# Kernel tuning notes

Measured on AMD Instinct MI355X. Metric: run time of the kernel, lower is better.

## Reference

```python
import jax, jax.numpy as jnp
import numpy as np

G_NUM, K_DEG = 3, 3  # grid intervals, spline order (module defaults)
LN_EPS = 1e-5


def _bspline_basis(x, grid, k):
    """Cox-de Boor B-spline basis. x: [N, D], grid: [D, G+2k+1] -> [N, D, G+k]."""
    xg = x[:, :, None]                      # [N, D, 1]
    g = grid[None, :, :]                    # [1, D, M]
    B = ((xg >= g[..., :-1]) & (xg < g[..., 1:])).astype(x.dtype)  # degree 0
    for d in range(1, k + 1):
        left = (xg - g[..., :-(d + 1)]) / (g[..., d:-1] - g[..., :-(d + 1)])
        right = (g[..., d + 1:] - xg) / (g[..., d + 1:] - g[..., 1:-d])
        B = left * B[..., :-1] + right * B[..., 1:]
    return B                                # [N, D, G+k]


def _kan_layer(x, grid, coef, scale_base, scale_sp, node_scale, node_bias):
    # spline branch: fold per-edge scale_sp into coef, contract basis without
    # materializing the [N, in, out] per-edge tensor
    basis = _bspline_basis(x, grid, K_DEG)              # [N, in, G+k]
    coef_eff = coef * scale_sp[..., None]               # [in, out, G+k]
    y = jnp.einsum('nib,iob->no', basis, coef_eff)      # spline sum over edges
    y = y + jax.nn.silu(x) @ scale_base                 # residual base function
    return node_scale * y + node_bias                   # per-node affine


def setup_inputs() -> dict:
    key = jax.random.key(0)
    ks = jax.random.split(key, 12)
    B, S = 16, 1024
    D0, D1, D2 = 256, 512, 256
    nb = G_NUM + K_DEG  # num basis fns = 6
    h = 2.0 / G_NUM
    knots = np.arange(-K_DEG, G_NUM + K_DEG + 1) * h - 1.0  # [G+2k+1]=10, range [-3,3]
    grid1 = jnp.asarray(np.tile(knots, (D0, 1)), jnp.float32)
    grid2 = jnp.asarray(np.tile(knots, (D1, 1)), jnp.float32)
    inp = {
        'x': jax.random.normal(ks[0], (B, S, D0), jnp.float32),
        'grid1': grid1,
        'coef1': jax.random.normal(ks[1], (D0, D1, nb), jnp.float32) * 0.1,
        'scale_base1': jax.random.normal(ks[2], (D0, D1), jnp.float32) / np.sqrt(D0),
        'scale_sp1': jnp.ones((D0, D1), jnp.float32),
        'node_scale1': jnp.ones((D1,), jnp.float32),
        'node_bias1': jnp.zeros((D1,), jnp.float32),
        'grid2': grid2,
        'coef2': jax.random.normal(ks[3], (D1, D2, nb), jnp.float32) * 0.1,
        'scale_base2': jax.random.normal(ks[4], (D1, D2), jnp.float32) / np.sqrt(D1),
        'scale_sp2': jnp.ones((D1, D2), jnp.float32),
        'node_scale2': jnp.ones((D2,), jnp.float32),
        'node_bias2': jnp.zeros((D2,), jnp.float32),
        'ln_gamma': jnp.ones((D2,), jnp.float32),
        'ln_beta': jnp.zeros((D2,), jnp.float32),
    }
    return inp


def reference(x, grid1, coef1, scale_base1, scale_sp1, node_scale1, node_bias1,
              grid2, coef2, scale_base2, scale_sp2, node_scale2, node_bias2,
              ln_gamma, ln_beta):
    b, s, d = x.shape
    residual = x  # start_dim == final_dim -> residual path active
    h = x.reshape(-1, d)
    h = _kan_layer(h, grid1, coef1, scale_base1, scale_sp1, node_scale1, node_bias1)
    h = _kan_layer(h, grid2, coef2, scale_base2, scale_sp2, node_scale2, node_bias2)
    h = h.reshape(b, s, -1)
    h = h + residual
    # LayerNorm over last dim
    mu = jnp.mean(h, axis=-1, keepdims=True)
    var = jnp.mean((h - mu) ** 2, axis=-1, keepdims=True)
    h = (h - mu) * jax.lax.rsqrt(var + LN_EPS) * ln_gamma + ln_beta
    # torch nn.GELU default is exact (erf) variant
    return jax.nn.gelu(h, approximate=False)
```

## Files before the change

kernel.cpp:

```cpp
#include <hip/hip_runtime.h>
#include <cstdint>
#include <cstddef>

using f16   = _Float16;
using half8 = __attribute__((ext_vector_type(8))) _Float16;
using f32x4 = __attribute__((ext_vector_type(4))) float;
using ull   = unsigned long long;

#define DINL __device__ __forceinline__

DINL void gload_lds16(const void* gptr, void* lptr) {
  __builtin_amdgcn_global_load_lds(
      reinterpret_cast<const __attribute__((address_space(1))) uint32_t*>(
          reinterpret_cast<uintptr_t>(gptr)),
      reinterpret_cast<__attribute__((address_space(3))) uint32_t*>(
          reinterpret_cast<uintptr_t>(lptr)),
      16, 0, 0);
}

DINL unsigned pkh(float a, float b) {
  unsigned short ha = __builtin_bit_cast(unsigned short, (f16)a);
  unsigned short hb = __builtin_bit_cast(unsigned short, (f16)b);
  return (unsigned)ha | ((unsigned)hb << 16);
}

struct U4 { unsigned x, y, z, w; };

DINL U4 expand_pack(float x) {
  float xs = (x + 3.0f) * 1.5f;
  float mf = floorf(xs);
  int   m  = (int)mf;
  float u = xs - mf, u2 = u * u, u3 = u2 * u, um = 1.0f - u;
  float p3 = u3 * (1.0f / 6.0f);
  float p2 = (1.0f + 3.0f * (u + u2 - u3)) * (1.0f / 6.0f);
  float p1 = (4.0f - 6.0f * u2 + 3.0f * u3) * (1.0f / 6.0f);
  float p0 = um * um * um * (1.0f / 6.0f);
  ull P = (ull)pkh(p0, p1) | ((ull)pkh(p2, p3) << 32);
  if ((unsigned)m > 8u) P = 0;
  int s    = m * 16 - 48;
  int sneg = min(63, max(0, -s));
  int spos = min(63, max(0, s));
  int shi2 = min(63, max(0, s - 64));
  ull rlo = (s < 0) ? (P >> sneg) : ((s < 64) ? (P << spos) : 0ull);
  ull rhi = (s < 0) ? 0ull
                    : ((s < 64) ? ((P >> (63 - spos)) >> 1) : (P << shi2));
  float sil = x / (1.0f + __expf(-x));
  U4 r;
  r.x = (unsigned)rlo;
  r.y = (unsigned)(rlo >> 32);
  r.z = (unsigned)rhi;
  r.w = pkh(sil, 0.0f);
  return r;
}

__global__ __launch_bounds__(256)
void prep_w_kernel(const float* __restrict__ coef, const float* __restrict__ ssp,
                   const float* __restrict__ sb, f16* __restrict__ Wt,
                   int Din, int Dout) {
  int idx = blockIdx.x * 256 + threadIdx.x;
  if (idx >= Din * Dout) return;
  int n = idx / Din;
  int d = idx - n * Din;
  float s = ssp[(size_t)d * Dout + n];
  const float* c = coef + ((size_t)d * Dout + n) * 6;
  half8 wv;
#pragma unroll
  for (int b = 0; b < 6; ++b) wv[b] = (f16)(c[b] * s);
  wv[6] = (f16)sb[(size_t)d * Dout + n];
  wv[7] = (f16)0.0f;
  int dp = (d & ~7) | ((d & 7) ^ (n & 7));
  *reinterpret_cast<half8*>(Wt + ((size_t)n * Din + dp) * 8) = wv;
}

template <bool BIAS>
__global__ __launch_bounds__(512, 2)
void kan_gemm(const float* __restrict__ X, int ldx,
              const f16* __restrict__ Wt, int ldw,
              const float* __restrict__ nscale, const float* __restrict__ nbias,
              int N, float* __restrict__ Out, int nsteps) {
  extern __shared__ char smem[];
  f16* bufA0 = (f16*)smem;
  f16* bufA1 = (f16*)(smem + 8192);
  f16* bufB0 = (f16*)(smem + 16384);
  f16* bufB1 = (f16*)(smem + 16384 + 32768);

  const int tid  = threadIdx.x;
  const int w    = tid >> 6;
  const int lane = tid & 63;
  const int l15  = lane & 15, l7 = lane & 7, hi = lane >> 4;
  const int wm   = w >> 2, wn = w & 3;
  const int m0   = blockIdx.y * 64;
  const int n0   = blockIdx.x * 256;
  const int dim0 = blockIdx.z * (nsteps * 8);
  float* outz = Out + (size_t)blockIdx.z * ((size_t)gridDim.y * 64) * N;

  const int ar = tid >> 3, ad = tid & 7;
  const float* asrc = X + (size_t)(m0 + ar) * ldx + dim0 + ad;
  const int aoff = ar * 64 + 8 * (ad ^ (ar & 7));

  const f16* wb[4];
  int ldsb[4];
#pragma unroll
  for (int q = 0; q < 4; ++q) {
    int c   = tid + q * 512;
    wb[q]   = Wt + (size_t)(n0 + (c >> 3)) * ldw + (size_t)dim0 * 8 + (c & 7) * 8;
    ldsb[q] = c * 8;
  }

  f32x4 acc[2][4] = {};

  auto stageB = [&](f16* buf, int k0) {
#pragma unroll
    for (int q = 0; q < 4; ++q) gload_lds16(wb[q] + k0, buf + ldsb[q]);
  };

  auto compute = [&](const f16* bA, const f16* bB) {
#pragma unroll
    for (int kk = 0; kk < 2; ++kk) {
      const int sl = kk * 4 + hi;
      half8 av[2], bv[4];
#pragma unroll
      for (int i = 0; i < 2; ++i)
        av[i] = *reinterpret_cast<const half8*>(
            bA + (wm * 32 + i * 16 + l15) * 64 + 8 * (sl ^ l7));
#pragma unroll
      for (int j = 0; j < 4; ++j)
        bv[j] = *reinterpret_cast<const half8*>(
            bB + (wn * 64 + j * 16 + l15) * 64 + 8 * (sl ^ l7));
#pragma unroll
      for (int i = 0; i < 2; ++i)
#pragma unroll
        for (int j = 0; j < 4; ++j)
          acc[i][j] = __builtin_amdgcn_mfma_f32_16x16x32_f16(av[i], bv[j], acc[i][j], 0, 0, 0);
    }
  };

  {
    float xv = asrc[0];
    stageB(bufB0, 0);
    U4 e = expand_pack(xv);
    *reinterpret_cast<U4*>(bufA0 + aoff) = e;
  }
  float xn = asrc[8];
  __syncthreads();

  for (int s = 0; s < nsteps; ++s) {
    const bool odd = s & 1;
    f16* curA = odd ? bufA1 : bufA0;
    f16* curB = odd ? bufB1 : bufB0;
    f16* nxtA = odd ? bufA0 : bufA1;
    f16* nxtB = odd ? bufB0 : bufB1;
    if (s + 1 < nsteps) stageB(nxtB, (s + 1) * 64);
    float xn2 = (s + 2 < nsteps) ? asrc[(size_t)(s + 2) * 8] : 0.0f;
    compute(curA, curB);
    if (s + 1 < nsteps) {
      U4 e = expand_pack(xn);
      *reinterpret_cast<U4*>(nxtA + aoff) = e;
    }
    xn = xn2;
    __syncthreads();
  }

#pragma unroll
  for (int j = 0; j < 4; ++j) {
    int col   = n0 + wn * 64 + j * 16 + l15;
    float nsv = nscale[col];
    float nbv = BIAS ? nbias[col] : 0.0f;
#pragma unroll
    for (int i = 0; i < 2; ++i) {
      int rb = m0 + wm * 32 + i * 16 + hi * 4;
#pragma unroll
      for (int r = 0; r < 4; ++r)
        outz[(size_t)(rb + r) * N + col] = nsv * acc[i][j][r] + nbv;
    }
  }
}

__global__ __launch_bounds__(256)
void ln_gelu_kernel(const float* __restrict__ P0, const float* __restrict__ P1,
                    const float* __restrict__ X,  const float* __restrict__ nb2,
                    const float* __restrict__ gamma, const float* __restrict__ beta,
                    float* __restrict__ out, int rows) {
  int row  = blockIdx.x * 4 + (threadIdx.x >> 6);
  int lane = threadIdx.x & 63;
  if (row >= rows) return;
  const float4 a  = *reinterpret_cast<const float4*>(P0 + (size_t)row * 256 + lane * 4);
  const float4 b  = *reinterpret_cast<const float4*>(P1 + (size_t)row * 256 + lane * 4);
  const float4 xr = *reinterpret_cast<const float4*>(X  + (size_t)row * 256 + lane * 4);
  const float4 nb = *reinterpret_cast<const float4*>(nb2 + lane * 4);
  const float4 g  = *reinterpret_cast<const float4*>(gamma + lane * 4);
  const float4 be = *reinterpret_cast<const float4*>(beta + lane * 4);
  float h[4] = { a.x + b.x + nb.x + xr.x, a.y + b.y + nb.y + xr.y,
                 a.z + b.z + nb.z + xr.z, a.w + b.w + nb.w + xr.w };
  float s = h[0] + h[1] + h[2] + h[3];
#pragma unroll
  for (int o = 32; o >= 1; o >>= 1) s += __shfl_xor(s, o);
  float mu = s * (1.0f / 256.0f);
  float vs = 0.f;
#pragma unroll
  for (int j = 0; j < 4; ++j) { float d = h[j] - mu; vs += d * d; }
#pragma unroll
  for (int o = 32; o >= 1; o >>= 1) vs += __shfl_xor(vs, o);
  float inv = rsqrtf(vs * (1.0f / 256.0f) + 1e-5f);
  float o4[4];
#pragma unroll
  for (int j = 0; j < 4; ++j) {
    float gj = (&g.x)[j], bj = (&be.x)[j];
    float v = (h[j] - mu) * inv * gj + bj;
    o4[j] = 0.5f * v * (1.0f + erff(v * 0.70710678118654752f));
  }
  *reinterpret_cast<float4*>(out + (size_t)row * 256 + lane * 4) =
      make_float4(o4[0], o4[1], o4[2], o4[3]);
}

extern "C" void kernel_launch(void* const* d_in, const int* in_sizes, int n_in,
                              void* d_out, int out_size, void* d_ws, size_t ws_size,
                              hipStream_t stream) {
  (void)in_sizes; (void)n_in; (void)out_size; (void)ws_size;
  const float* x     = (const float*)d_in[0];
  const float* coef1 = (const float*)d_in[2];
  const float* sb1   = (const float*)d_in[3];
  const float* ssp1  = (const float*)d_in[4];
  const float* ns1   = (const float*)d_in[5];
  const float* nb1   = (const float*)d_in[6];
  const float* coef2 = (const float*)d_in[8];
  const float* sb2   = (const float*)d_in[9];
  const float* ssp2  = (const float*)d_in[10];
  const float* ns2   = (const float*)d_in[11];
  const float* nb2   = (const float*)d_in[12];
  const float* lgam  = (const float*)d_in[13];
  const float* lbet  = (const float*)d_in[14];
  float* out = (float*)d_out;

  const int Ntok = 16 * 1024;
  const int D0 = 256, D1 = 512, D2 = 256;

  char*  ws   = (char*)d_ws;
  float* h1   = (float*)ws;
  size_t off  = (size_t)Ntok * D1 * sizeof(float);
  float* part = (float*)(ws + off);
  off += (size_t)2 * Ntok * D2 * sizeof(float);
  f16* Wt1 = (f16*)(ws + off);
  off += (size_t)D1 * D0 * 8 * sizeof(f16);
  f16* Wt2 = (f16*)(ws + off);

  prep_w_kernel<<<(D0 * D1 + 255) / 256, 256, 0, stream>>>(coef1, ssp1, sb1, Wt1, D0, D1);
  prep_w_kernel<<<(D1 * D2 + 255) / 256, 256, 0, stream>>>(coef2, ssp2, sb2, Wt2, D1, D2);

  kan_gemm<true><<<dim3(D1 / 256, Ntok / 64, 1), 512, 81920, stream>>>(
      x, D0, Wt1, D0 * 8, ns1, nb1, D1, h1, D0 / 8);

  kan_gemm<false><<<dim3(D2 / 256, Ntok / 64, 2), 512, 81920, stream>>>(
      h1, D1, Wt2, D1 * 8, ns2, nullptr, D2, part, D1 / 16);

  ln_gelu_kernel<<<Ntok / 4, 256, 0, stream>>>(
      part, part + (size_t)Ntok * D2, x, nb2, lgam, lbet, out, Ntok);
}
```

Before: 126.0 us.

## Use static LDS buffers, unroll double-buffer loop by two, raise occupancy bound

Replaces the dynamic shared-memory allocation with static LDS arrays and unrolls the double-buffered main loop in pairs, so buffer selection is compile-time and the per-step ternaries go away. Launch bounds change from 2 to 4 blocks per multiprocessor, which caps registers per thread harder and may cause spills. The static LDS also drops from the 80KB dynamic request to 80KB of actual arrays (same size), so the occupancy gain depends on the LDS limit. The loop assumes an even step count of at least 2.

After: 123.8 us. Within noise of the previous version (-1.7%).

```diff
diff --git a/kernel.cpp b/kernel.cpp
--- a/kernel.cpp
+++ b/kernel.cpp
@@ -73,16 +73,15 @@
 }
 
 template <bool BIAS>
-__global__ __launch_bounds__(512, 2)
+__global__ __launch_bounds__(512, 4)
 void kan_gemm(const float* __restrict__ X, int ldx,
               const f16* __restrict__ Wt, int ldw,
               const float* __restrict__ nscale, const float* __restrict__ nbias,
               int N, float* __restrict__ Out, int nsteps) {
-  extern __shared__ char smem[];
-  f16* bufA0 = (f16*)smem;
-  f16* bufA1 = (f16*)(smem + 8192);
-  f16* bufB0 = (f16*)(smem + 16384);
-  f16* bufB1 = (f16*)(smem + 16384 + 32768);
+  __shared__ alignas(16) f16 A0[64 * 64];
+  __shared__ alignas(16) f16 A1[64 * 64];
+  __shared__ alignas(16) f16 B0[256 * 64];
+  __shared__ alignas(16) f16 B1[256 * 64];
 
   const int tid  = threadIdx.x;
   const int w    = tid >> 6;
@@ -135,31 +134,41 @@
     }
   };
 
+  auto writeA = [&](f16* buf, U4 e) {
+    *reinterpret_cast<U4*>(buf + aoff) = e;
+  };
+
   {
-    float xv = asrc[0];
-    stageB(bufB0, 0);
-    U4 e = expand_pack(xv);
-    *reinterpret_cast<U4*>(bufA0 + aoff) = e;
+    float xa = asrc[0];
+    stageB(B0, 0);
+    writeA(A0, expand_pack(xa));
   }
   float xn = asrc[8];
   __syncthreads();
 
-  for (int s = 0; s < nsteps; ++s) {
-    const bool odd = s & 1;
-    f16* curA = odd ? bufA1 : bufA0;
-    f16* curB = odd ? bufB1 : bufB0;
-    f16* nxtA = odd ? bufA0 : bufA1;
-    f16* nxtB = odd ? bufB0 : bufB1;
-    if (s + 1 < nsteps) stageB(nxtB, (s + 1) * 64);
-    float xn2 = (s + 2 < nsteps) ? asrc[(size_t)(s + 2) * 8] : 0.0f;
-    compute(curA, curB);
-    if (s + 1 < nsteps) {
-      U4 e = expand_pack(xn);
-      *reinterpret_cast<U4*>(nxtA + aoff) = e;
-    }
-    xn = xn2;
+  const float* ap = asrc + 16;
+  const int npairs = (nsteps - 2) >> 1;
+  int k = 64;
+  for (int p = 0; p < npairs; ++p) {
+    stageB(B1, k);
+    float xa2 = ap[0];
+    compute(A0, B0);
+    writeA(A1, expand_pack(xn));
     __syncthreads();
-  }
+    stageB(B0, k + 64);
+    xn = ap[8];
+    compute(A1, B1);
+    writeA(A0, expand_pack(xa2));
+    __syncthreads();
+    ap += 16;
+    k  += 128;
+  }
+
+  stageB(B1, k);
+  compute(A0, B0);
+  writeA(A1, expand_pack(xn));
+  __syncthreads();
+  compute(A1, B1);
 
 #pragma unroll
   for (int j = 0; j < 4; ++j) {
@@ -247,10 +256,10 @@
   prep_w_kernel<<<(D0 * D1 + 255) / 256, 256, 0, stream>>>(coef1, ssp1, sb1, Wt1, D0, D1);
   prep_w_kernel<<<(D1 * D2 + 255) / 256, 256, 0, stream>>>(coef2, ssp2, sb2, Wt2, D1, D2);
 
-  kan_gemm<true><<<dim3(D1 / 256, Ntok / 64, 1), 512, 81920, stream>>>(
+  kan_gemm<true><<<dim3(D1 / 256, Ntok / 64, 1), 512, 0, stream>>>(
       x, D0, Wt1, D0 * 8, ns1, nb1, D1, h1, D0 / 8);
 
-  kan_gemm<false><<<dim3(D2 / 256, Ntok / 64, 2), 512, 81920, stream>>>(
+  kan_gemm<false><<<dim3(D2 / 256, Ntok / 64, 2), 512, 0, stream>>>(
       h1, D1, Wt2, D1 * 8, ns2, nullptr, D2, part, D1 / 16);
 
   ln_gelu_kernel<<<Ntok / 4, 256, 0, stream>>>(
```
